# Kernel optimization log

Hardware: AMD Instinct MI355X
Metric: run time of the kernel (lower is better)

Reference implementation:

```python
import jax, jax.numpy as jnp
import numpy as np

B, T, D, E, C = 4, 4096, 2048, 8, 1024
H = D // E  # per-expert hidden = out_features // num_experts = 256


def setup_inputs() -> dict:
    key = jax.random.key(0)
    ks = jax.random.split(key, 7)
    x = jax.random.normal(ks[0], (B, T, D), dtype=jnp.float32)
    # nn.Linear-style init scale ~ 1/sqrt(fan_in)
    W1 = jax.random.normal(ks[1], (E, H, D), dtype=jnp.float32) / np.sqrt(D)
    b1 = jax.random.normal(ks[2], (E, H), dtype=jnp.float32) / np.sqrt(D)
    W2 = jax.random.normal(ks[3], (E, D, H), dtype=jnp.float32) / np.sqrt(D)
    b2 = jax.random.normal(ks[4], (D,), dtype=jnp.float32) / np.sqrt(D)
    expert_indices = jax.random.randint(ks[5], (B, E, C), 0, T, dtype=jnp.int32)
    expert_gate = jax.random.uniform(ks[6], (B, E, C), dtype=jnp.float32)
    return {"x": x, "W1": W1, "b1": b1, "W2": W2, "b2": b2,
            "expert_indices": expert_indices, "expert_gate": expert_gate,
            "num_tokens": T}


def reference(x, W1, b1, W2, b2, expert_indices, expert_gate, num_tokens):
    # x: (B,T,D); expert_indices/expert_gate: (B,E,C)
    Bb = x.shape[0]
    Ee, Cc = expert_indices.shape[1], expert_indices.shape[2]
    b_idx = jnp.arange(Bb)[:, None, None]
    # dispatch: gather tokens per expert -> (B,E,C,D)
    sel = x[b_idx, expert_indices]
    # contract: per-expert GEMM -> (B,E,C,H)
    h = jnp.einsum('becd,ehd->bech', sel, W1) + b1[None, :, None, :]
    h = jax.nn.gelu(h, approximate=False)
    # expand: per-expert GEMM -> (B,E,C,D), shared output bias
    y = jnp.einsum('bech,eoh->beco', h, W2) + b2
    y = y * expert_gate[..., None]
    # combine: gated scatter-add back to token positions -> (B,T,D)
    out = jnp.zeros((Bb, num_tokens, x.shape[2]), dtype=x.dtype)
    out = out.at[jnp.arange(Bb)[:, None], expert_indices.reshape(Bb, Ee * Cc)].add(
        y.reshape(Bb, Ee * Cc, -1))
    return out
```

## Files before the change

kernel.cpp:

```cpp
#include <hip/hip_runtime.h>
#include <hip/hip_bf16.h>
#include <math.h>

#define B_ 4
#define T_ 4096
#define D_ 2048
#define E_ 8
#define C_ 1024
#define H_ 256
#define SLOTCAP 32

typedef unsigned short u16;
typedef unsigned long long u64;
typedef __attribute__((ext_vector_type(8))) short short8;
typedef __attribute__((ext_vector_type(4))) float f32x4;

__device__ __forceinline__ u16 f2bf_n(float f) {
    union { __hip_bfloat16 b; u16 u; } v;
    v.b = __float2bfloat16(f);
    return v.u;
}
__device__ __forceinline__ float bf2f(u16 u) {
    union { unsigned u; float f; } v; v.u = ((unsigned)u) << 16;
    return v.f;
}

__device__ __forceinline__ int swz(int row, int chunk) {
    return (row << 6) + ((chunk ^ (row & 7)) << 3);
}

__device__ __forceinline__ void gload16(const void* g, void* l) {
    __builtin_amdgcn_global_load_lds(
        (const __attribute__((address_space(1))) void*)g,
        (__attribute__((address_space(3))) void*)l, 16, 0, 0);
}

__global__ __launch_bounds__(256) void conv_w1_img(
    const float* __restrict__ W1, u16* __restrict__ img)
{
    const int cid = blockIdx.x * 256 + threadIdx.x;
    const int e = cid >> 16;
    const int kt = (cid >> 11) & 31;
    const int row = (cid >> 3) & 255;
    const int sc = cid & 7;
    const float* s = W1 + (((size_t)e * 256 + row) * 2048 + kt * 64
                           + ((sc ^ (row & 7)) << 3));
    f32x4 v0 = *reinterpret_cast<const f32x4*>(s);
    f32x4 v1 = *reinterpret_cast<const f32x4*>(s + 4);
    u16 o[8];
    #pragma unroll
    for (int j = 0; j < 4; ++j) { o[j] = f2bf_n(v0[j]); o[j + 4] = f2bf_n(v1[j]); }
    *reinterpret_cast<short8*>(img + (size_t)cid * 8) =
        *reinterpret_cast<const short8*>(o);
}

__global__ __launch_bounds__(256) void conv_w2_img(
    const float* __restrict__ W2, u16* __restrict__ img)
{
    const int cid = blockIdx.x * 256 + threadIdx.x;
    const int e = cid >> 16;
    const int nt = (cid >> 13) & 7;
    const int kt = (cid >> 11) & 3;
    const int row = (cid >> 3) & 255;
    const int sc = cid & 7;
    const float* s = W2 + (((size_t)e * 2048 + nt * 256 + row) * 256 + kt * 64
                           + ((sc ^ (row & 7)) << 3));
    f32x4 v0 = *reinterpret_cast<const f32x4*>(s);
    f32x4 v1 = *reinterpret_cast<const f32x4*>(s + 4);
    u16 o[8];
    #pragma unroll
    for (int j = 0; j < 4; ++j) { o[j] = f2bf_n(v0[j]); o[j + 4] = f2bf_n(v1[j]); }
    *reinterpret_cast<short8*>(img + (size_t)cid * 8) =
        *reinterpret_cast<const short8*>(o);
}

__global__ __launch_bounds__(256) void zero_cnt(int* __restrict__ cnt)
{
    const int i = (blockIdx.x * 256 + threadIdx.x) * 4;
    *reinterpret_cast<f32x4*>(cnt + i) = (f32x4){0.f, 0.f, 0.f, 0.f};
}

__global__ __launch_bounds__(512) void gemm1_v10(
    const float* __restrict__ x, const u16* __restrict__ W1img,
    const float* __restrict__ b1, const int* __restrict__ idx,
    u16* __restrict__ Himg)
{
    const int be = blockIdx.x;
    const int mt = blockIdx.y;
    const int b = be >> 3, e = be & 7;
    const int m0 = mt * 64;

    __shared__ __align__(16) u16 As[2][4096];
    __shared__ __align__(16) u16 Bs[2][16384];

    const int tid = threadIdx.x;
    const int lane = tid & 63, wid = tid >> 6;
    const int wm = wid >> 2, wn = wid & 3;
    const int l15 = lane & 15, lk = lane >> 4;

    const int row8 = tid >> 3, asc = tid & 7;
    const int tok = idx[(b * E_ + e) * C_ + m0 + row8];
    const float* aRow = x + ((size_t)b * T_ + tok) * D_ + asc * 8;
    const int aOff = swz(row8, asc);

    const u16* bSrc = W1img + (size_t)e * 32 * 16384 + (size_t)tid * 8;
    const int wofs = wid * 512;

    f32x4 pa0, pa1;

#define A_LOAD(t)                                                             \
    do {                                                                      \
        pa0 = *reinterpret_cast<const f32x4*>(aRow + (t) * 64);               \
        pa1 = *reinterpret_cast<const f32x4*>(aRow + (t) * 64 + 4);           \
    } while (0)

#define A_WRITE(buf)                                                          \
    do {                                                                      \
        short8 s;                                                             \
        _Pragma("unroll")                                                     \
        for (int r = 0; r < 4; ++r) {                                         \
            s[r] = (short)f2bf_n(pa0[r]); s[r + 4] = (short)f2bf_n(pa1[r]);   \
        }                                                                     \
        *reinterpret_cast<short8*>(&As[buf][aOff]) = s;                       \
    } while (0)

#define B_ISSUE(buf, t)                                                       \
    do {                                                                      \
        const u16* b_ = bSrc + (size_t)(t) * 16384;                           \
        gload16(b_,         &Bs[buf][wofs]);                                  \
        gload16(b_ + 4096,  &Bs[buf][4096 + wofs]);                           \
        gload16(b_ + 8192,  &Bs[buf][8192 + wofs]);                           \
        gload16(b_ + 12288, &Bs[buf][12288 + wofs]);                          \
    } while (0)

    f32x4 acc[2][4];
    #pragma unroll
    for (int i = 0; i < 2; ++i)
        #pragma unroll
        for (int j = 0; j < 4; ++j)
            acc[i][j] = (f32x4){0.f, 0.f, 0.f, 0.f};

    A_LOAD(0); A_WRITE(0);
    A_LOAD(1); A_WRITE(1);
    B_ISSUE(0, 0);
    B_ISSUE(1, 1);
    A_LOAD(2);
    asm volatile("s_waitcnt lgkmcnt(0)" ::: "memory");

    const int NT = D_ / 64;
    for (int t = 0; t < NT; ++t) {
        const int cur = t & 1;
        if (t < NT - 1) asm volatile("s_waitcnt vmcnt(6)" ::: "memory");
        else            asm volatile("s_waitcnt vmcnt(0)" ::: "memory");
        __builtin_amdgcn_s_barrier();
        __builtin_amdgcn_sched_barrier(0);
        #pragma unroll
        for (int kk = 0; kk < 2; ++kk) {
            short8 af[2], bfr[4];
            #pragma unroll
            for (int m = 0; m < 2; ++m) {
                const int row = wm * 32 + m * 16 + l15;
                af[m] = *reinterpret_cast<const short8*>(
                    &As[cur][swz(row, kk * 4 + lk)]);
            }
            #pragma unroll
            for (int n = 0; n < 4; ++n) {
                const int row = wn * 64 + n * 16 + l15;
                bfr[n] = *reinterpret_cast<const short8*>(
                    &Bs[cur][swz(row, kk * 4 + lk)]);
            }
            __builtin_amdgcn_s_setprio(1);
            #pragma unroll
            for (int m = 0; m < 2; ++m)
                #pragma unroll
                for (int n = 0; n < 4; ++n)
                    acc[m][n] = __builtin_amdgcn_mfma_f32_16x16x32_bf16(
                        bfr[n], af[m], acc[m][n], 0, 0, 0);
            __builtin_amdgcn_s_setprio(0);
        }
        asm volatile("s_waitcnt lgkmcnt(0)" ::: "memory");
        __builtin_amdgcn_s_barrier();
        __builtin_amdgcn_sched_barrier(0);
        if (t + 2 < NT) A_WRITE(cur);
        if (t + 3 < NT) A_LOAD(t + 3);
        if (t + 2 < NT) B_ISSUE(cur, t + 2);
    }
#undef A_LOAD
#undef A_WRITE
#undef B_ISSUE

    const size_t hblk = ((size_t)(be * 16 + mt) * 4 + wn) * 4096;
    #pragma unroll
    for (int m = 0; m < 2; ++m) {
        const int row = wm * 32 + m * 16 + l15;
        #pragma unroll
        for (int n = 0; n < 4; ++n) {
            const int hb = wn * 64 + n * 16 + lk * 4;
            f32x4 bias = *reinterpret_cast<const f32x4*>(&b1[e * H_ + hb]);
            u16 o[4];
            #pragma unroll
            for (int r = 0; r < 4; ++r) {
                float h = acc[m][n][r] + bias[r];
                float g = 0.5f * h * (1.0f + erff(h * 0.70710678118f));
                o[r] = f2bf_n(g);
            }
            const int lc = (n * 2 + (lk >> 1)) ^ (row & 7);
            u16* p = Himg + hblk + row * 64 + lc * 8 + (lk & 1) * 4;
            *reinterpret_cast<u64*>(p) = *reinterpret_cast<const u64*>(o);
        }
    }
}

__global__ __launch_bounds__(512) void gemm2_v8(
    const u16* __restrict__ Himg, const u16* __restrict__ W2img,
    const float* __restrict__ b2, const float* __restrict__ gate,
    u16* __restrict__ Ybuf)
{
    const int be = blockIdx.x;
    const int nt = blockIdx.y;
    const int b = be >> 3, e = be & 7;
    const int n0 = nt * 256;

    __shared__ __align__(16) u16 As[16384];
    __shared__ __align__(16) u16 Bs[65536];

    const int tid = threadIdx.x;
    const int lane = tid & 63, wid = tid >> 6;
    const int wm = wid >> 2, wn = wid & 3;
    const int l15 = lane & 15, lk = lane >> 4;
    const int wofs = wid * 512;

    const u16* bPanel = W2img + (size_t)(e * 8 + nt) * 65536;
    #pragma unroll
    for (int j = 0; j < 16; ++j)
        gload16(bPanel + (size_t)(j * 512 + tid) * 8, &Bs[j * 4096 + wofs]);

    const u16* aBase = Himg + (size_t)(be * 16) * 16384 + (size_t)tid * 8;

#define A_ISSUE(mt)                                                           \
    do {                                                                      \
        const u16* a_ = aBase + (size_t)(mt) * 16384;                         \
        gload16(a_,          &As[wofs]);                                      \
        gload16(a_ + 4096,   &As[4096 + wofs]);                               \
        gload16(a_ + 8192,   &As[8192 + wofs]);                               \
        gload16(a_ + 12288,  &As[12288 + wofs]);                              \
    } while (0)

    A_ISSUE(0);

    f32x4 bias[4];
    #pragma unroll
    for (int n = 0; n < 4; ++n)
        bias[n] = *reinterpret_cast<const f32x4*>(
            &b2[n0 + wn * 64 + n * 16 + lk * 4]);

    const int gbase = (b * E_ + e) * C_ + wm * 32 + l15;
    const size_t ybase = (size_t)(b * E_ + e) * C_;

    float gc0 = gate[gbase];
    float gc1 = gate[gbase + 16];

    asm volatile("s_waitcnt vmcnt(0)" ::: "memory");
    __builtin_amdgcn_s_barrier();
    __builtin_amdgcn_sched_barrier(0);

    for (int mt = 0; mt < 16; ++mt) {
        f32x4 acc[2][4];
        #pragma unroll
        for (int i = 0; i < 2; ++i)
            #pragma unroll
            for (int j = 0; j < 4; ++j)
                acc[i][j] = (f32x4){0.f, 0.f, 0.f, 0.f};

        #pragma unroll
        for (int t = 0; t < 4; ++t) {
            #pragma unroll
            for (int kk = 0; kk < 2; ++kk) {
                short8 af[2], bfr[4];
                #pragma unroll
                for (int m = 0; m < 2; ++m) {
                    const int row = wm * 32 + m * 16 + l15;
                    af[m] = *reinterpret_cast<const short8*>(
                        &As[t * 4096 + swz(row, kk * 4 + lk)]);
                }
                #pragma unroll
                for (int n = 0; n < 4; ++n) {
                    const int row = wn * 64 + n * 16 + l15;
                    bfr[n] = *reinterpret_cast<const short8*>(
                        &Bs[t * 16384 + swz(row, kk * 4 + lk)]);
                }
                __builtin_amdgcn_s_setprio(1);
                #pragma unroll
                for (int m = 0; m < 2; ++m)
                    #pragma unroll
                    for (int n = 0; n < 4; ++n)
                        acc[m][n] = __builtin_amdgcn_mfma_f32_16x16x32_bf16(
                            bfr[n], af[m], acc[m][n], 0, 0, 0);
                __builtin_amdgcn_s_setprio(0);
            }
        }

        asm volatile("s_waitcnt lgkmcnt(0)" ::: "memory");
        __builtin_amdgcn_s_barrier();
        __builtin_amdgcn_sched_barrier(0);

        if (mt < 15) A_ISSUE(mt + 1);
        float gn0 = 0.f, gn1 = 0.f;
        if (mt < 15) {
            gn0 = gate[gbase + (mt + 1) * 64];
            gn1 = gate[gbase + (mt + 1) * 64 + 16];
        }

        #pragma unroll
        for (int m = 0; m < 2; ++m) {
            const int cl = wm * 32 + m * 16 + l15;
            const float g = (m == 0) ? gc0 : gc1;
            u16* rowp = Ybuf + (ybase + mt * 64 + cl) * (size_t)D_ + n0;
            #pragma unroll
            for (int n = 0; n < 4; ++n) {
                const int db = wn * 64 + n * 16 + lk * 4;
                u16 o[4];
                #pragma unroll
                for (int r = 0; r < 4; ++r)
                    o[r] = f2bf_n((acc[m][n][r] + bias[n][r]) * g);
                *reinterpret_cast<u64*>(rowp + db) =
                    *reinterpret_cast<const u64*>(o);
            }
        }

        if (mt < 15) {
            asm volatile("s_waitcnt vmcnt(18)" ::: "memory");
            __builtin_amdgcn_s_barrier();
            __builtin_amdgcn_sched_barrier(0);
        }
        gc0 = gn0; gc1 = gn1;
    }
#undef A_ISSUE
}

__global__ __launch_bounds__(256) void fill_kernel(
    const int* __restrict__ idx, int* __restrict__ cnt,
    int* __restrict__ slots)
{
    int i = blockIdx.x * 256 + threadIdx.x;
    if (i >= B_ * E_ * C_) return;
    int b = i / (E_ * C_);
    int slot = i % (E_ * C_);
    int t = idx[i];
    int p = atomicAdd(&cnt[b * T_ + t], 1);
    if (p < SLOTCAP) slots[(b * T_ + t) * SLOTCAP + p] = slot;
}

__global__ __launch_bounds__(256) void combine_kernel(
    const u16* __restrict__ Ybuf, const int* __restrict__ cnt,
    const int* __restrict__ slots, float* __restrict__ out)
{
    const int bt = blockIdx.x;
    const int tid = threadIdx.x;
    __shared__ int sl[SLOTCAP];
    int n = cnt[bt];
    n = n > SLOTCAP ? SLOTCAP : n;
    if (tid < n) sl[tid] = slots[bt * SLOTCAP + tid];
    __syncthreads();
    const int b = bt >> 12;
    float a[8] = {0.f, 0.f, 0.f, 0.f, 0.f, 0.f, 0.f, 0.f};
    for (int s = 0; s < n; ++s) {
        const u16* yrow = Ybuf + ((size_t)b * (E_ * C_) + sl[s]) * D_ + tid * 8;
        short8 v = *reinterpret_cast<const short8*>(yrow);
        #pragma unroll
        for (int j = 0; j < 8; ++j) a[j] += bf2f((u16)v[j]);
    }
    float* orow = out + (size_t)bt * D_ + tid * 8;
    *reinterpret_cast<f32x4*>(orow)     = (f32x4){a[0], a[1], a[2], a[3]};
    *reinterpret_cast<f32x4*>(orow + 4) = (f32x4){a[4], a[5], a[6], a[7]};
}

extern "C" void kernel_launch(void* const* d_in, const int* in_sizes, int n_in,
                              void* d_out, int out_size, void* d_ws, size_t ws_size,
                              hipStream_t stream) {
    const float* x    = (const float*)d_in[0];
    const float* W1   = (const float*)d_in[1];
    const float* b1   = (const float*)d_in[2];
    const float* W2   = (const float*)d_in[3];
    const float* b2   = (const float*)d_in[4];
    const int*   idx  = (const int*)d_in[5];
    const float* gate = (const float*)d_in[6];
    float* out = (float*)d_out;

    const size_t nW = (size_t)E_ * H_ * D_;
    const size_t nH = (size_t)B_ * E_ * C_ * H_;
    const size_t nY = (size_t)B_ * E_ * C_ * D_;

    u16* W1img = (u16*)d_ws;
    u16* W2img = W1img + nW;
    u16* Himg  = W2img + nW;
    u16* Ybuf  = Himg + nH;
    int* cnt   = (int*)(Ybuf + nY);
    int* slots = cnt + (size_t)B_ * T_;

    zero_cnt<<<(B_ * T_) / 1024, 256, 0, stream>>>(cnt);
    conv_w1_img<<<2048, 256, 0, stream>>>(W1, W1img);
    conv_w2_img<<<2048, 256, 0, stream>>>(W2, W2img);
    fill_kernel<<<(B_ * E_ * C_) / 256, 256, 0, stream>>>(idx, cnt, slots);

    gemm1_v10<<<dim3(32, 16), 512, 0, stream>>>(x, W1img, b1, idx, Himg);
    gemm2_v8<<<dim3(32, 8), 512, 0, stream>>>(Himg, W2img, b2, gate, Ybuf);
    combine_kernel<<<B_ * T_, 256, 0, stream>>>(Ybuf, cnt, slots, out);
}
```

Baseline: 212.0 us.

## Halve gemm1 block to 4 waves with larger per-wave tiles

The first expert GEMM now runs 256 threads (4 waves) per block instead of 512. Each wave computes a 64x64 output tile (4x4 MFMA fragments) over the full 64-row M tile, and each thread loads twice as much A and B data per stage; the vmcnt threshold is adjusted to match. The intent is more operand reuse per wave, fewer LDS reads per MFMA, and two resident blocks per CU via launch_bounds(256,2). The cost is higher register pressure from the larger accumulator and prefetch buffers, and fewer waves to hide latency.

```diff
diff --git a/kernel.cpp b/kernel.cpp
--- a/kernel.cpp
+++ b/kernel.cpp
@@ -80,7 +80,7 @@
     *reinterpret_cast<f32x4*>(cnt + i) = (f32x4){0.f, 0.f, 0.f, 0.f};
 }
 
-__global__ __launch_bounds__(512) void gemm1_v10(
+__global__ __launch_bounds__(256, 2) void gemm1_v11(
     const float* __restrict__ x, const u16* __restrict__ W1img,
     const float* __restrict__ b1, const int* __restrict__ idx,
     u16* __restrict__ Himg)
@@ -95,47 +95,49 @@
 
     const int tid = threadIdx.x;
     const int lane = tid & 63, wid = tid >> 6;
-    const int wm = wid >> 2, wn = wid & 3;
     const int l15 = lane & 15, lk = lane >> 4;
 
-    const int row8 = tid >> 3, asc = tid & 7;
+    const int row8 = tid >> 2, sc2 = (tid & 3) * 2;
     const int tok = idx[(b * E_ + e) * C_ + m0 + row8];
-    const float* aRow = x + ((size_t)b * T_ + tok) * D_ + asc * 8;
-    const int aOff = swz(row8, asc);
-
-    const u16* bSrc = W1img + (size_t)e * 32 * 16384 + (size_t)tid * 8;
-    const int wofs = wid * 512;
-
-    f32x4 pa0, pa1;
+    const float* aRow = x + ((size_t)b * T_ + tok) * D_ + sc2 * 8;
+    const int aOff0 = swz(row8, sc2), aOff1 = swz(row8, sc2 + 1);
+
+    const u16* bSrcLane = W1img + (size_t)e * 32 * 16384 + wid * 512 + lane * 8;
+    const int bofs = wid * 512;
+
+    f32x4 pa[4];
 
 #define A_LOAD(t)                                                             \
     do {                                                                      \
-        pa0 = *reinterpret_cast<const f32x4*>(aRow + (t) * 64);               \
-        pa1 = *reinterpret_cast<const f32x4*>(aRow + (t) * 64 + 4);           \
+        pa[0] = *reinterpret_cast<const f32x4*>(aRow + (t) * 64);             \
+        pa[1] = *reinterpret_cast<const f32x4*>(aRow + (t) * 64 + 4);         \
+        pa[2] = *reinterpret_cast<const f32x4*>(aRow + (t) * 64 + 8);         \
+        pa[3] = *reinterpret_cast<const f32x4*>(aRow + (t) * 64 + 12);        \
     } while (0)
 
 #define A_WRITE(buf)                                                          \
     do {                                                                      \
-        short8 s;                                                             \
+        short8 s0, s1;                                                        \
         _Pragma("unroll")                                                     \
         for (int r = 0; r < 4; ++r) {                                         \
-            s[r] = (short)f2bf_n(pa0[r]); s[r + 4] = (short)f2bf_n(pa1[r]);   \
+            s0[r] = (short)f2bf_n(pa[0][r]); s0[r + 4] = (short)f2bf_n(pa[1][r]); \
+            s1[r] = (short)f2bf_n(pa[2][r]); s1[r + 4] = (short)f2bf_n(pa[3][r]); \
         }                                                                     \
-        *reinterpret_cast<short8*>(&As[buf][aOff]) = s;                       \
+        *reinterpret_cast<short8*>(&As[buf][aOff0]) = s0;                     \
+        *reinterpret_cast<short8*>(&As[buf][aOff1]) = s1;                     \
     } while (0)
 
 #define B_ISSUE(buf, t)                                                       \
     do {                                                                      \
-        const u16* b_ = bSrc + (size_t)(t) * 16384;                           \
-        gload16(b_,         &Bs[buf][wofs]);                                  \
-        gload16(b_ + 4096,  &Bs[buf][4096 + wofs]);                           \
-        gload16(b_ + 8192,  &Bs[buf][8192 + wofs]);                           \
-        gload16(b_ + 12288, &Bs[buf][12288 + wofs]);                          \
+        const u16* b_ = bSrcLane + (size_t)(t) * 16384;                       \
+        _Pragma("unroll")                                                     \
+        for (int j = 0; j < 8; ++j)                                           \
+            gload16(b_ + j * 2048, &Bs[buf][j * 2048 + bofs]);                \
     } while (0)
 
-    f32x4 acc[2][4];
-    #pragma unroll
-    for (int i = 0; i < 2; ++i)
+    f32x4 acc[4][4];
+    #pragma unroll
+    for (int i = 0; i < 4; ++i)
         #pragma unroll
         for (int j = 0; j < 4; ++j)
             acc[i][j] = (f32x4){0.f, 0.f, 0.f, 0.f};
@@ -150,28 +152,28 @@
     const int NT = D_ / 64;
     for (int t = 0; t < NT; ++t) {
         const int cur = t & 1;
-        if (t < NT - 1) asm volatile("s_waitcnt vmcnt(6)" ::: "memory");
+        if (t < NT - 1) asm volatile("s_waitcnt vmcnt(12)" ::: "memory");
         else            asm volatile("s_waitcnt vmcnt(0)" ::: "memory");
         __builtin_amdgcn_s_barrier();
         __builtin_amdgcn_sched_barrier(0);
         #pragma unroll
         for (int kk = 0; kk < 2; ++kk) {
-            short8 af[2], bfr[4];
-            #pragma unroll
-            for (int m = 0; m < 2; ++m) {
-                const int row = wm * 32 + m * 16 + l15;
+            short8 af[4], bfr[4];
+            #pragma unroll
+            for (int m = 0; m < 4; ++m) {
+                const int row = m * 16 + l15;
                 af[m] = *reinterpret_cast<const short8*>(
                     &As[cur][swz(row, kk * 4 + lk)]);
             }
             #pragma unroll
             for (int n = 0; n < 4; ++n) {
-                const int row = wn * 64 + n * 16 + l15;
+                const int row = wid * 64 + n * 16 + l15;
                 bfr[n] = *reinterpret_cast<const short8*>(
                     &Bs[cur][swz(row, kk * 4 + lk)]);
             }
             __builtin_amdgcn_s_setprio(1);
             #pragma unroll
-            for (int m = 0; m < 2; ++m)
+            for (int m = 0; m < 4; ++m)
                 #pragma unroll
                 for (int n = 0; n < 4; ++n)
                     acc[m][n] = __builtin_amdgcn_mfma_f32_16x16x32_bf16(
@@ -189,13 +191,13 @@
 #undef A_WRITE
 #undef B_ISSUE
 
-    const size_t hblk = ((size_t)(be * 16 + mt) * 4 + wn) * 4096;
-    #pragma unroll
-    for (int m = 0; m < 2; ++m) {
-        const int row = wm * 32 + m * 16 + l15;
+    const size_t hblk = ((size_t)(be * 16 + mt) * 4 + wid) * 4096;
+    #pragma unroll
+    for (int m = 0; m < 4; ++m) {
+        const int row = m * 16 + l15;
         #pragma unroll
         for (int n = 0; n < 4; ++n) {
-            const int hb = wn * 64 + n * 16 + lk * 4;
+            const int hb = wid * 64 + n * 16 + lk * 4;
             f32x4 bias = *reinterpret_cast<const f32x4*>(&b1[e * H_ + hb]);
             u16 o[4];
             #pragma unroll
@@ -403,7 +405,7 @@
     conv_w2_img<<<2048, 256, 0, stream>>>(W2, W2img);
     fill_kernel<<<(B_ * E_ * C_) / 256, 256, 0, stream>>>(idx, cnt, slots);
 
-    gemm1_v10<<<dim3(32, 16), 512, 0, stream>>>(x, W1img, b1, idx, Himg);
+    gemm1_v11<<<dim3(32, 16), 256, 0, stream>>>(x, W1img, b1, idx, Himg);
     gemm2_v8<<<dim3(32, 8), 512, 0, stream>>>(Himg, W2img, b2, gate, Ybuf);
     combine_kernel<<<B_ * T_, 256, 0, stream>>>(Ybuf, cnt, slots, out);
 }
```

Result: slower. 219.0 us (+3.3%).

## Double-buffer A tiles in gemm2 with 32-row halves and per-wave column strips

Applied to the files above, without the earlier changes.

Restructures the second expert GEMM so the A (hidden activation) tile is split into 32-row halves held in a two-slot LDS ring. The next half is prefetched before the current MFMA loop runs, instead of after a barrier that follows compute. The warp layout changes from 2x4 (M by N) to 1x8, with each wave owning a 32-column strip over all 32 rows. This cuts the per-step barrier stall and hides global latency better, but it doubles the number of loop iterations and barriers and gives each wave less MFMA work per B-fragment load.

```diff
diff --git a/kernel.cpp b/kernel.cpp
--- a/kernel.cpp
+++ b/kernel.cpp
@@ -211,7 +211,7 @@
     }
 }
 
-__global__ __launch_bounds__(512) void gemm2_v8(
+__global__ __launch_bounds__(512) void gemm2_v9(
     const u16* __restrict__ Himg, const u16* __restrict__ W2img,
     const float* __restrict__ b2, const float* __restrict__ gate,
     u16* __restrict__ Ybuf)
@@ -221,12 +221,11 @@
     const int b = be >> 3, e = be & 7;
     const int n0 = nt * 256;
 
-    __shared__ __align__(16) u16 As[16384];
+    __shared__ __align__(16) u16 As[2][8192];
     __shared__ __align__(16) u16 Bs[65536];
 
     const int tid = threadIdx.x;
     const int lane = tid & 63, wid = tid >> 6;
-    const int wm = wid >> 2, wn = wid & 3;
     const int l15 = lane & 15, lk = lane >> 4;
     const int wofs = wid * 512;
 
@@ -235,26 +234,30 @@
     for (int j = 0; j < 16; ++j)
         gload16(bPanel + (size_t)(j * 512 + tid) * 8, &Bs[j * 4096 + wofs]);
 
-    const u16* aBase = Himg + (size_t)(be * 16) * 16384 + (size_t)tid * 8;
-
-#define A_ISSUE(mt)                                                           \
+    const int r0 = wid * 2, r1 = wid * 2 + 1;
+    const int kt0 = r0 >> 2, sub0 = r0 & 3;
+    const int kt1 = r1 >> 2, sub1 = r1 & 3;
+    const u16* aTile = Himg + (size_t)(be * 16) * 16384;
+
+#define A_ISSUE(buf, mtp)                                                     \
     do {                                                                      \
-        const u16* a_ = aBase + (size_t)(mt) * 16384;                         \
-        gload16(a_,          &As[wofs]);                                      \
-        gload16(a_ + 4096,   &As[4096 + wofs]);                               \
-        gload16(a_ + 8192,   &As[8192 + wofs]);                               \
-        gload16(a_ + 12288,  &As[12288 + wofs]);                              \
+        const int mt_ = (mtp) >> 1, h_ = (mtp) & 1;                           \
+        const u16* base_ = aTile + (size_t)mt_ * 16384 + h_ * 2048;           \
+        gload16(base_ + (size_t)kt0 * 4096 + sub0 * 512 + lane * 8,           \
+                &As[buf][r0 * 512]);                                          \
+        gload16(base_ + (size_t)kt1 * 4096 + sub1 * 512 + lane * 8,           \
+                &As[buf][r1 * 512]);                                          \
     } while (0)
 
-    A_ISSUE(0);
-
-    f32x4 bias[4];
-    #pragma unroll
-    for (int n = 0; n < 4; ++n)
+    A_ISSUE(0, 0);
+
+    f32x4 bias[2];
+    #pragma unroll
+    for (int n = 0; n < 2; ++n)
         bias[n] = *reinterpret_cast<const f32x4*>(
-            &b2[n0 + wn * 64 + n * 16 + lk * 4]);
-
-    const int gbase = (b * E_ + e) * C_ + wm * 32 + l15;
+            &b2[n0 + wid * 32 + n * 16 + lk * 4]);
+
+    const int gbase = (b * E_ + e) * C_ + l15;
     const size_t ybase = (size_t)(b * E_ + e) * C_;
 
     float gc0 = gate[gbase];
@@ -264,28 +267,38 @@
     __builtin_amdgcn_s_barrier();
     __builtin_amdgcn_sched_barrier(0);
 
-    for (int mt = 0; mt < 16; ++mt) {
-        f32x4 acc[2][4];
+    const int NMT = 32;
+    for (int mtp = 0; mtp < NMT; ++mtp) {
+        const int cur = mtp & 1;
+
+        if (mtp + 1 < NMT) A_ISSUE(cur ^ 1, mtp + 1);
+        float gn0 = 0.f, gn1 = 0.f;
+        if (mtp + 1 < NMT) {
+            gn0 = gate[gbase + (mtp + 1) * 32];
+            gn1 = gate[gbase + (mtp + 1) * 32 + 16];
+        }
+
+        f32x4 acc[2][2];
         #pragma unroll
         for (int i = 0; i < 2; ++i)
             #pragma unroll
-            for (int j = 0; j < 4; ++j)
+            for (int j = 0; j < 2; ++j)
                 acc[i][j] = (f32x4){0.f, 0.f, 0.f, 0.f};
 
         #pragma unroll
         for (int t = 0; t < 4; ++t) {
             #pragma unroll
             for (int kk = 0; kk < 2; ++kk) {
-                short8 af[2], bfr[4];
+                short8 af[2], bfr[2];
                 #pragma unroll
                 for (int m = 0; m < 2; ++m) {
-                    const int row = wm * 32 + m * 16 + l15;
+                    const int rh = m * 16 + l15;
                     af[m] = *reinterpret_cast<const short8*>(
-                        &As[t * 4096 + swz(row, kk * 4 + lk)]);
+                        &As[cur][t * 2048 + swz(rh, kk * 4 + lk)]);
                 }
                 #pragma unroll
-                for (int n = 0; n < 4; ++n) {
-                    const int row = wn * 64 + n * 16 + l15;
+                for (int n = 0; n < 2; ++n) {
+                    const int row = wid * 32 + n * 16 + l15;
                     bfr[n] = *reinterpret_cast<const short8*>(
                         &Bs[t * 16384 + swz(row, kk * 4 + lk)]);
                 }
@@ -293,32 +306,21 @@
                 #pragma unroll
                 for (int m = 0; m < 2; ++m)
                     #pragma unroll
-                    for (int n = 0; n < 4; ++n)
+                    for (int n = 0; n < 2; ++n)
                         acc[m][n] = __builtin_amdgcn_mfma_f32_16x16x32_bf16(
                             bfr[n], af[m], acc[m][n], 0, 0, 0);
                 __builtin_amdgcn_s_setprio(0);
             }
         }
 
-        asm volatile("s_waitcnt lgkmcnt(0)" ::: "memory");
-        __builtin_amdgcn_s_barrier();
-        __builtin_amdgcn_sched_barrier(0);
-
-        if (mt < 15) A_ISSUE(mt + 1);
-        float gn0 = 0.f, gn1 = 0.f;
-        if (mt < 15) {
-            gn0 = gate[gbase + (mt + 1) * 64];
-            gn1 = gate[gbase + (mt + 1) * 64 + 16];
-        }
-
         #pragma unroll
         for (int m = 0; m < 2; ++m) {
-            const int cl = wm * 32 + m * 16 + l15;
+            const int cl = m * 16 + l15;
             const float g = (m == 0) ? gc0 : gc1;
-            u16* rowp = Ybuf + (ybase + mt * 64 + cl) * (size_t)D_ + n0;
-            #pragma unroll
-            for (int n = 0; n < 4; ++n) {
-                const int db = wn * 64 + n * 16 + lk * 4;
+            u16* rowp = Ybuf + (ybase + mtp * 32 + cl) * (size_t)D_ + n0;
+            #pragma unroll
+            for (int n = 0; n < 2; ++n) {
+                const int db = wid * 32 + n * 16 + lk * 4;
                 u16 o[4];
                 #pragma unroll
                 for (int r = 0; r < 4; ++r)
@@ -327,13 +329,14 @@
                     *reinterpret_cast<const u64*>(o);
             }
         }
-
-        if (mt < 15) {
-            asm volatile("s_waitcnt vmcnt(18)" ::: "memory");
+        gc0 = gn0; gc1 = gn1;
+
+        if (mtp + 1 < NMT) {
+            asm volatile("s_waitcnt lgkmcnt(0)" ::: "memory");
+            asm volatile("s_waitcnt vmcnt(6)" ::: "memory");
             __builtin_amdgcn_s_barrier();
             __builtin_amdgcn_sched_barrier(0);
         }
-        gc0 = gn0; gc1 = gn1;
     }
 #undef A_ISSUE
 }
@@ -404,6 +407,6 @@
     fill_kernel<<<(B_ * E_ * C_) / 256, 256, 0, stream>>>(idx, cnt, slots);
 
     gemm1_v10<<<dim3(32, 16), 512, 0, stream>>>(x, W1img, b1, idx, Himg);
-    gemm2_v8<<<dim3(32, 8), 512, 0, stream>>>(Himg, W2img, b2, gate, Ybuf);
+    gemm2_v9<<<dim3(32, 8), 512, 0, stream>>>(Himg, W2img, b2, gate, Ybuf);
     combine_kernel<<<B_ * T_, 256, 0, stream>>>(Ybuf, cnt, slots, out);
 }
```

New measurement: 221.6 us. 4.5% more time.
